# Optimization experiments

Measured on AMD Instinct MI355X. Metric: run time of the kernel, lower is better.

## Reference

```python
import jax, jax.numpy as jnp
import numpy as np

HEAD_SIZE = 1024
NUM_HEADS = 8
D_K = HEAD_SIZE // NUM_HEADS  # only used as the softmax scale; no head split in this module
B, S = 8, 2048


def setup_inputs() -> dict:
    key = jax.random.key(0)
    ks = jax.random.split(key, 11)
    d = HEAD_SIZE
    scale = 1.0 / np.sqrt(d)
    inp = {
        'query': jax.random.normal(ks[0], (B, S, d), dtype=jnp.float32),
        'key': jax.random.normal(ks[1], (B, S, d), dtype=jnp.float32),
        'value': jax.random.normal(ks[2], (B, S, d), dtype=jnp.float32),
        'Wq': jax.random.normal(ks[3], (d, d), dtype=jnp.float32) * scale,
        'bq': jnp.zeros((d,), dtype=jnp.float32),
        'Wk': jax.random.normal(ks[4], (d, d), dtype=jnp.float32) * scale,
        'bk': jnp.zeros((d,), dtype=jnp.float32),
        'Wv': jax.random.normal(ks[5], (d, d), dtype=jnp.float32) * scale,
        'bv': jnp.zeros((d,), dtype=jnp.float32),
        'Wo': jax.random.normal(ks[6], (d, d), dtype=jnp.float32) * scale,
        'bo': jnp.zeros((d,), dtype=jnp.float32),
    }
    return inp


def reference(query, key, value, Wq, bq, Wk, bk, Wv, bv, Wo, bo):
    # per-input linear projections (torch Linear: x @ W.T + b)
    q = jnp.einsum('bsd,ed->bse', query, Wq) + bq
    k = jnp.einsum('bsd,ed->bse', key, Wk) + bk
    v = jnp.einsum('bsd,ed->bse', value, Wv) + bv
    # NOTE: no head split in the original module; scale uses d_k = head_size/num_heads
    scores = jnp.einsum('bqd,bkd->bqk', q, k) / jnp.sqrt(jnp.float32(D_K))
    p_attn = jax.nn.softmax(scores, axis=-1)  # [B, S, S]
    x = jnp.einsum('bqk,bkd->bqd', p_attn, v)
    out = jnp.einsum('bsd,ed->bse', x, Wo) + bo
    return out
```

## Files before the change

kernel.cpp:

```cpp
#include <hip/hip_runtime.h>
#include <hip/hip_bf16.h>
#include <math.h>

typedef __bf16 bf16_t;
typedef _Float16 f16_t;
typedef bf16_t bf16x8 __attribute__((ext_vector_type(8)));
typedef bf16_t bf16x4 __attribute__((ext_vector_type(4)));
typedef f16_t  f16x8  __attribute__((ext_vector_type(8)));
typedef f16_t  f16x4  __attribute__((ext_vector_type(4)));
typedef float  f32x4  __attribute__((ext_vector_type(4)));

__global__ __launch_bounds__(256) void cvt_f32_bf16(
    const float* __restrict__ in, bf16_t* __restrict__ out, int n4) {
  int i = blockIdx.x * 256 + threadIdx.x;
  if (i >= n4) return;
  float4 v = ((const float4*)in)[i];
  bf16x4 o;
  o[0] = (bf16_t)v.x; o[1] = (bf16_t)v.y; o[2] = (bf16_t)v.z; o[3] = (bf16_t)v.w;
  ((bf16x4*)out)[i] = o;
}

__global__ __launch_bounds__(256) void transpose_bf16(
    const bf16_t* __restrict__ in, bf16_t* __restrict__ out, int R, int C) {
  __shared__ bf16_t t[64][65];
  size_t boff = (size_t)blockIdx.z * R * C;
  in += boff; out += boff;
  int r0 = blockIdx.y * 64, c0 = blockIdx.x * 64;
  int x = threadIdx.x & 63, y4 = threadIdx.x >> 6;
  #pragma unroll
  for (int yy = y4; yy < 64; yy += 4)
    t[yy][x] = in[(size_t)(r0 + yy) * C + c0 + x];
  __syncthreads();
  #pragma unroll
  for (int yy = y4; yy < 64; yy += 4)
    out[(size_t)(c0 + yy) * R + r0 + x] = t[x][yy];
}

__global__ __launch_bounds__(256) void softmax_rows_f16(f16_t* __restrict__ sc) {
  f16_t* rp = sc + (size_t)blockIdx.x * 2048;
  int tid = threadIdx.x;
  f16x8 v = ((const f16x8*)rp)[tid];
  float f[8];
  #pragma unroll
  for (int t = 0; t < 8; t++) f[t] = (float)v[t];

  float m = f[0];
  #pragma unroll
  for (int t = 1; t < 8; t++) m = fmaxf(m, f[t]);
  #pragma unroll
  for (int o = 32; o; o >>= 1) m = fmaxf(m, __shfl_xor(m, o));
  __shared__ float redm[4];
  if ((tid & 63) == 0) redm[tid >> 6] = m;
  __syncthreads();
  m = fmaxf(fmaxf(redm[0], redm[1]), fmaxf(redm[2], redm[3]));

  float s = 0.f;
  #pragma unroll
  for (int t = 0; t < 8; t++) { f[t] = __expf(f[t] - m); s += f[t]; }
  #pragma unroll
  for (int o = 32; o; o >>= 1) s += __shfl_xor(s, o);
  __shared__ float reds[4];
  if ((tid & 63) == 0) reds[tid >> 6] = s;
  __syncthreads();
  s = reds[0] + reds[1] + reds[2] + reds[3];
  float inv = 1.0f / s;

  bf16x8 o8;
  #pragma unroll
  for (int t = 0; t < 8; t++) o8[t] = (bf16_t)(f[t] * inv);
  ((bf16x8*)rp)[tid] = o8;
}

__device__ __forceinline__ void store4(float* p, float4 v) { *(float4*)p = v; }
__device__ __forceinline__ void store4(bf16_t* p, float4 v) {
  bf16x4 o; o[0] = (bf16_t)v.x; o[1] = (bf16_t)v.y;
  o[2] = (bf16_t)v.z; o[3] = (bf16_t)v.w; *(bf16x4*)p = o;
}
__device__ __forceinline__ void store4(f16_t* p, float4 v) {
  f16x4 o; o[0] = (f16_t)v.x; o[1] = (f16_t)v.y;
  o[2] = (f16_t)v.z; o[3] = (f16_t)v.w; *(f16x4*)p = o;
}

#define BM 256
#define BN 256
#define BK 64

__device__ __forceinline__ void load16_lds(const bf16_t* g, bf16_t* l) {
  __builtin_amdgcn_global_load_lds(
      (__attribute__((address_space(1))) void*)const_cast<bf16_t*>(g),
      (__attribute__((address_space(3))) void*)l, 16, 0, 0);
}

template <typename CT>
__global__ __launch_bounds__(512, 2) void gemm256(
    const bf16_t* __restrict__ A, int lda, size_t strA,
    const bf16_t* __restrict__ B, int ldb, size_t strB,
    CT* __restrict__ C, int ldc, size_t strC,
    const float* __restrict__ bias, float scale,
    int K, int batch_on_x) {
  __shared__ __align__(16) char smem[10][16384];
  char* smem0 = &smem[0][0];

  int bz, mt, nt;
  if (batch_on_x) { bz = blockIdx.x; nt = blockIdx.y; mt = blockIdx.z; }
  else            { mt = blockIdx.x; nt = blockIdx.y; bz = blockIdx.z; }
  A += (size_t)bz * strA;
  B += (size_t)bz * strB;
  C += (size_t)bz * strC;
  int m0 = mt * BM, n0 = nt * BN;
  int tid  = threadIdx.x;
  int lane = tid & 63, wv = tid >> 6;
  int wrow = wv >> 2;
  int wcol = wv & 3;

  f32x4 acc[8][4];
  #pragma unroll
  for (int i = 0; i < 8; i++)
    #pragma unroll
    for (int j = 0; j < 4; j++) acc[i][j] = (f32x4)0.f;

  int lrow = lane & 15;
  int lk8  = (lane >> 4) * 8;
  int xm   = (lrow & 8) << 2;

  auto rd = [&](const char* half, int blk, int kcol) -> bf16x8 {
    int byte = (((blk << 1) + (kcol >> 5)) << 10)
             + (lrow << 6) + (((kcol & 31) << 1) ^ xm);
    return *(const bf16x8*)(half + byte);
  };

  auto stage_half = [&](int h, int slot) {
    int th = h >> 2, hf = h & 3;
    char* dstb = smem0 + slot * 16384;
    const bf16_t* g; int rb, ld;
    if (hf < 2) { g = A; rb = m0 + hf * 128;       ld = lda; }
    else        { g = B; rb = n0 + (hf - 2) * 128; ld = ldb; }
    int k0 = th * BK;
    #pragma unroll
    for (int q = 0; q < 2; q++) {
      int l = q * 8192 + wv * 1024 + lane * 16;
      int inner = l & 1023, s = l >> 10;
      int rl   = ((s >> 1) << 4) | (inner >> 6);
      int colb = (inner & 63) ^ (((inner >> 9) & 1) << 5);
      int col  = ((s & 1) << 5) | (colb >> 1);
      load16_lds(g + (size_t)(rb + rl) * ld + k0 + col,
                 (bf16_t*)(dstb + q * 8192 + wv * 1024));
    }
  };

  int nk = K / BK;
  int nh = 4 * nk;
  int bl = (wcol & 1) * 4;

  #pragma unroll
  for (int h = 0; h < 8; ++h)
    if (h < nh) stage_half(h, h);
  asm volatile("s_waitcnt vmcnt(8)" ::: "memory");
  asm volatile("s_barrier" ::: "memory");

  bf16x8 a0[4][2], a1[4][2], bb[2][2];
  {
    const char* Ah0 = smem0 + (0 + wrow) * 16384;
    const char* Bh0 = smem0 + (2 + (wcol >> 1)) * 16384;
    #pragma unroll
    for (int i = 0; i < 4; ++i)
      #pragma unroll
      for (int s = 0; s < 2; ++s)
        a0[i][s] = rd(Ah0, i, s * 32 + lk8);
    #pragma unroll
    for (int j = 0; j < 2; ++j)
      #pragma unroll
      for (int s = 0; s < 2; ++s)
        bb[j][s] = rd(Bh0, bl + j, s * 32 + lk8);
  }

  int rs = 0;
  int ss = 8;

  for (int t = 0; t < nk; ++t) {
    int hb = 4 * t + 8;
    int sa  = rs + wrow;
    int sb  = rs + 2 + (wcol >> 1); if (sb  >= 10) sb  -= 10;
    int san = rs + 4 + wrow;        if (san >= 10) san -= 10;
    int sbn = rs + 6 + (wcol >> 1); if (sbn >= 10) sbn -= 10;
    const char* Ah  = smem0 + sa  * 16384;
    const char* Bh  = smem0 + sb  * 16384;
    const char* Ahn = smem0 + san * 16384;
    const char* Bhn = smem0 + sbn * 16384;

    #pragma unroll
    for (int i = 0; i < 4; ++i)
      #pragma unroll
      for (int s = 0; s < 2; ++s)
        a1[i][s] = rd(Ah, 4 + i, s * 32 + lk8);
    if (hb + 0 < nh) { stage_half(hb + 0, ss); ss = (ss == 9) ? 0 : ss + 1; }
    asm volatile("s_barrier" ::: "memory");
    __builtin_amdgcn_s_setprio(1);
    #pragma unroll
    for (int i = 0; i < 4; ++i)
      #pragma unroll
      for (int j = 0; j < 2; ++j)
        #pragma unroll
        for (int s = 0; s < 2; ++s)
          acc[i][j] = __builtin_amdgcn_mfma_f32_16x16x32_bf16(
              a0[i][s], bb[j][s], acc[i][j], 0, 0, 0);
    __builtin_amdgcn_s_setprio(0);
    asm volatile("s_barrier" ::: "memory");

    if (hb + 1 < nh) { stage_half(hb + 1, ss); ss = (ss == 9) ? 0 : ss + 1; }
    asm volatile("s_barrier" ::: "memory");
    __builtin_amdgcn_s_setprio(1);
    #pragma unroll
    for (int i = 0; i < 4; ++i)
      #pragma unroll
      for (int j = 0; j < 2; ++j)
        #pragma unroll
        for (int s = 0; s < 2; ++s)
          acc[4 + i][j] = __builtin_amdgcn_mfma_f32_16x16x32_bf16(
              a1[i][s], bb[j][s], acc[4 + i][j], 0, 0, 0);
    __builtin_amdgcn_s_setprio(0);
    asm volatile("s_barrier" ::: "memory");

    #pragma unroll
    for (int j = 0; j < 2; ++j)
      #pragma unroll
      for (int s = 0; s < 2; ++s)
        bb[j][s] = rd(Bh, bl + 2 + j, s * 32 + lk8);
    if (hb + 2 < nh) { stage_half(hb + 2, ss); ss = (ss == 9) ? 0 : ss + 1; }
    if (t <= nk - 3) asm volatile("s_waitcnt vmcnt(6)" ::: "memory");
    else             asm volatile("s_waitcnt vmcnt(0)" ::: "memory");
    asm volatile("s_barrier" ::: "memory");
    __builtin_amdgcn_s_setprio(1);
    #pragma unroll
    for (int i = 0; i < 4; ++i)
      #pragma unroll
      for (int j = 0; j < 2; ++j)
        #pragma unroll
        for (int s = 0; s < 2; ++s)
          acc[4 + i][2 + j] = __builtin_amdgcn_mfma_f32_16x16x32_bf16(
              a1[i][s], bb[j][s], acc[4 + i][2 + j], 0, 0, 0);
    __builtin_amdgcn_s_setprio(0);
    asm volatile("s_barrier" ::: "memory");

    if (hb + 3 < nh) { stage_half(hb + 3, ss); ss = (ss == 9) ? 0 : ss + 1; }
    asm volatile("s_barrier" ::: "memory");
    __builtin_amdgcn_s_setprio(1);
    #pragma unroll
    for (int i = 0; i < 4; ++i)
      #pragma unroll
      for (int j = 0; j < 2; ++j)
        #pragma unroll
        for (int s = 0; s < 2; ++s)
          acc[i][2 + j] = __builtin_amdgcn_mfma_f32_16x16x32_bf16(
              a0[i][s], bb[j][s], acc[i][2 + j], 0, 0, 0);
    __builtin_amdgcn_s_setprio(0);
    if (t + 1 < nk) {
      #pragma unroll
      for (int j = 0; j < 2; ++j)
        #pragma unroll
        for (int s = 0; s < 2; ++s)
          bb[j][s] = rd(Bhn, bl + j, s * 32 + lk8);
      #pragma unroll
      for (int i = 0; i < 4; ++i)
        #pragma unroll
        for (int s = 0; s < 2; ++s)
          a0[i][s] = rd(Ahn, i, s * 32 + lk8);
    }
    asm volatile("s_barrier" ::: "memory");

    rs += 4; if (rs >= 10) rs -= 10;
  }

  float* Cs = (float*)smem0;
  #pragma unroll
  for (int q = 0; q < 4; ++q) {
    __syncthreads();
    if (wrow == (q >> 1)) {
      #pragma unroll
      for (int ii = 0; ii < 4; ++ii) {
        int i = (q & 1) * 4 + ii;
        int lr = ii * 16 + (lane >> 4) * 4;
        #pragma unroll
        for (int j = 0; j < 4; ++j) {
          int lc = wcol * 64 + j * 16 + (lane & 15);
          #pragma unroll
          for (int r = 0; r < 4; ++r)
            Cs[(lr + r) * 260 + lc] = acc[i][j][r];
        }
      }
    }
    __syncthreads();
    #pragma unroll
    for (int io = 0; io < 8; ++io) {
      int idx = io * 512 + tid;
      int r = idx >> 6, c4 = (idx & 63) * 4;
      float4 v = *(const float4*)&Cs[r * 260 + c4];
      int grow = m0 + q * 64 + r;
      int gcol = n0 + c4;
      float4 bv = bias ? *(const float4*)&bias[gcol] : make_float4(0, 0, 0, 0);
      v.x = v.x * scale + bv.x; v.y = v.y * scale + bv.y;
      v.z = v.z * scale + bv.z; v.w = v.w * scale + bv.w;
      store4(C + (size_t)grow * ldc + gcol, v);
    }
  }
}

extern "C" void kernel_launch(void* const* d_in, const int* in_sizes, int n_in,
                              void* d_out, int out_size, void* d_ws, size_t ws_size,
                              hipStream_t stream) {
  const float* query = (const float*)d_in[0];
  const float* key_  = (const float*)d_in[1];
  const float* value = (const float*)d_in[2];
  const float* Wq = (const float*)d_in[3];
  const float* bq = (const float*)d_in[4];
  const float* Wk = (const float*)d_in[5];
  const float* bk = (const float*)d_in[6];
  const float* Wv = (const float*)d_in[7];
  const float* bv = (const float*)d_in[8];
  const float* Wo = (const float*)d_in[9];
  const float* bo = (const float*)d_in[10];
  float* out = (float*)d_out;

  const int Bb = 8, S = 2048, D = 1024;
  const int MS = Bb * S;
  const size_t ND = (size_t)MS * D;
  const size_t WD = (size_t)D * D;

  char* ws = (char*)d_ws;
  bf16_t* Wqb = (bf16_t*)ws;
  bf16_t* Wkb = Wqb + WD;
  bf16_t* Wvb = Wkb + WD;
  bf16_t* Wob = Wvb + WD;
  f16_t*  SC  = (f16_t*)(Wob + WD);
  bf16_t* IN  = (bf16_t*)SC;
  bf16_t* Qb  = (bf16_t*)((char*)SC + (size_t)Bb * S * S * 2);
  bf16_t* Kb  = Qb + ND;
  bf16_t* VT  = Kb;
  bf16_t* Xb  = Kb + ND;

  const int n4i = (int)(ND / 4), n4w = (int)(WD / 4);
  dim3 blk(512);

  cvt_f32_bf16<<<dim3(n4w / 256), 256, 0, stream>>>(Wq, Wqb, n4w);
  cvt_f32_bf16<<<dim3(n4w / 256), 256, 0, stream>>>(Wk, Wkb, n4w);
  cvt_f32_bf16<<<dim3(n4w / 256), 256, 0, stream>>>(Wv, Wvb, n4w);
  cvt_f32_bf16<<<dim3(n4w / 256), 256, 0, stream>>>(Wo, Wob, n4w);

  dim3 pgrid(MS / BM, D / BN, 1);
  cvt_f32_bf16<<<dim3(n4i / 256), 256, 0, stream>>>(query, IN, n4i);
  gemm256<bf16_t><<<pgrid, blk, 0, stream>>>(
      IN, D, 0, Wqb, D, 0, Qb, D, 0, bq, 1.f, D, 0);
  cvt_f32_bf16<<<dim3(n4i / 256), 256, 0, stream>>>(key_, IN, n4i);
  gemm256<bf16_t><<<pgrid, blk, 0, stream>>>(
      IN, D, 0, Wkb, D, 0, Kb, D, 0, bk, 1.f, D, 0);
  cvt_f32_bf16<<<dim3(n4i / 256), 256, 0, stream>>>(value, IN, n4i);
  gemm256<bf16_t><<<pgrid, blk, 0, stream>>>(
      IN, D, 0, Wvb, D, 0, Xb, D, 0, bv, 1.f, D, 0);

  gemm256<f16_t><<<dim3(Bb, S / BN, S / BM), blk, 0, stream>>>(
      Qb, D, (size_t)S * D, Kb, D, (size_t)S * D, SC, S, (size_t)S * S,
      nullptr, 0.08838834764831845f, D, 1);

  transpose_bf16<<<dim3(D / 64, S / 64, Bb), 256, 0, stream>>>(Xb, VT, S, D);

  softmax_rows_f16<<<dim3(Bb * S), 256, 0, stream>>>(SC);

  gemm256<bf16_t><<<dim3(Bb, D / BN, S / BM), blk, 0, stream>>>(
      (const bf16_t*)SC, S, (size_t)S * S, VT, S, (size_t)D * S,
      Xb, D, (size_t)S * D, nullptr, 1.f, S, 1);

  gemm256<float><<<pgrid, blk, 0, stream>>>(
      Xb, D, 0, Wob, D, 0, out, D, 0, bo, 1.f, D, 0);
}
```

Before: 572.9 us.

## Fuse fp32-to-bf16 input conversion and V transpose into projection GEMMs

The projection GEMMs now load fp32 activations straight from global memory into registers, convert them to bf16 and write them into LDS. This removes the three separate conversion kernels and their round trips through a bf16 workspace. The V projection writes its output transposed from the epilogue, which removes the separate transpose kernel, and the four weight conversions are merged into one launch. In exchange, A-tile staging now goes through registers instead of direct-to-LDS loads, which adds register pressure and changes the pipeline wait counts. The transposed epilogue also does strided reads from shared memory.

```diff
diff --git a/kernel.cpp b/kernel.cpp
--- a/kernel.cpp
+++ b/kernel.cpp
@@ -10,30 +10,18 @@
 typedef f16_t  f16x4  __attribute__((ext_vector_type(4)));
 typedef float  f32x4  __attribute__((ext_vector_type(4)));
 
-__global__ __launch_bounds__(256) void cvt_f32_bf16(
-    const float* __restrict__ in, bf16_t* __restrict__ out, int n4) {
+__global__ __launch_bounds__(256) void cvt_w4(
+    const float* __restrict__ w0, const float* __restrict__ w1,
+    const float* __restrict__ w2, const float* __restrict__ w3,
+    bf16_t* __restrict__ out, int n4) {
+  const float* src = blockIdx.y == 0 ? w0 : blockIdx.y == 1 ? w1
+                   : blockIdx.y == 2 ? w2 : w3;
   int i = blockIdx.x * 256 + threadIdx.x;
   if (i >= n4) return;
-  float4 v = ((const float4*)in)[i];
+  float4 v = ((const float4*)src)[i];
   bf16x4 o;
   o[0] = (bf16_t)v.x; o[1] = (bf16_t)v.y; o[2] = (bf16_t)v.z; o[3] = (bf16_t)v.w;
-  ((bf16x4*)out)[i] = o;
-}
-
-__global__ __launch_bounds__(256) void transpose_bf16(
-    const bf16_t* __restrict__ in, bf16_t* __restrict__ out, int R, int C) {
-  __shared__ bf16_t t[64][65];
-  size_t boff = (size_t)blockIdx.z * R * C;
-  in += boff; out += boff;
-  int r0 = blockIdx.y * 64, c0 = blockIdx.x * 64;
-  int x = threadIdx.x & 63, y4 = threadIdx.x >> 6;
-  #pragma unroll
-  for (int yy = y4; yy < 64; yy += 4)
-    t[yy][x] = in[(size_t)(r0 + yy) * C + c0 + x];
-  __syncthreads();
-  #pragma unroll
-  for (int yy = y4; yy < 64; yy += 4)
-    out[(size_t)(c0 + yy) * R + r0 + x] = t[x][yy];
+  ((bf16x4*)(out + (size_t)blockIdx.y * n4 * 4))[i] = o;
 }
 
 __global__ __launch_bounds__(256) void softmax_rows_f16(f16_t* __restrict__ sc) {
@@ -91,9 +79,9 @@
       (__attribute__((address_space(3))) void*)l, 16, 0, 0);
 }
 
-template <typename CT>
+template <typename CT, bool AF32, bool TOUT>
 __global__ __launch_bounds__(512, 2) void gemm256(
-    const bf16_t* __restrict__ A, int lda, size_t strA,
+    const void* __restrict__ Av, int lda, size_t strA,
     const bf16_t* __restrict__ B, int ldb, size_t strB,
     CT* __restrict__ C, int ldc, size_t strC,
     const float* __restrict__ bias, float scale,
@@ -104,7 +92,8 @@
   int bz, mt, nt;
   if (batch_on_x) { bz = blockIdx.x; nt = blockIdx.y; mt = blockIdx.z; }
   else            { mt = blockIdx.x; nt = blockIdx.y; bz = blockIdx.z; }
-  A += (size_t)bz * strA;
+  const bf16_t* A16 = (const bf16_t*)Av + (AF32 ? 0 : (size_t)bz * strA);
+  const float*  A32 = (const float*)Av + (AF32 ? (size_t)bz * strA : 0);
   B += (size_t)bz * strB;
   C += (size_t)bz * strC;
   int m0 = mt * BM, n0 = nt * BN;
@@ -129,13 +118,8 @@
     return *(const bf16x8*)(half + byte);
   };
 
-  auto stage_half = [&](int h, int slot) {
-    int th = h >> 2, hf = h & 3;
+  auto stage_g = [&](const bf16_t* g, int rb, int ld, int k0, int slot) {
     char* dstb = smem0 + slot * 16384;
-    const bf16_t* g; int rb, ld;
-    if (hf < 2) { g = A; rb = m0 + hf * 128;       ld = lda; }
-    else        { g = B; rb = n0 + (hf - 2) * 128; ld = ldb; }
-    int k0 = th * BK;
     #pragma unroll
     for (int q = 0; q < 2; q++) {
       int l = q * 8192 + wv * 1024 + lane * 16;
@@ -148,15 +132,69 @@
     }
   };
 
+  auto ldA32 = [&](int th, int hf, f32x4* r) {
+    #pragma unroll
+    for (int q = 0; q < 2; q++) {
+      int sub  = q * 8 + wv;
+      int grow = hf * 128 + (sub >> 1) * 16 + (lane >> 2);
+      int gcol = (sub & 1) * 32 + (lane & 3) * 8;
+      const float* gp = A32 + (size_t)(m0 + grow) * lda + th * BK + gcol;
+      r[2 * q]     = *(const f32x4*)gp;
+      r[2 * q + 1] = *(const f32x4*)(gp + 4);
+    }
+  };
+  auto wrA = [&](const f32x4* r, int slot) {
+    char* db = smem0 + slot * 16384;
+    #pragma unroll
+    for (int q = 0; q < 2; q++) {
+      int dl  = q * 8192 + wv * 1024 + lane * 16;
+      int dst = dl ^ (((dl >> 9) & 1) << 5);
+      bf16x8 o;
+      #pragma unroll
+      for (int e = 0; e < 4; e++) {
+        o[e]     = (bf16_t)r[2 * q][e];
+        o[4 + e] = (bf16_t)r[2 * q + 1][e];
+      }
+      *(bf16x8*)(db + dst) = o;
+    }
+  };
+
   int nk = K / BK;
-  int nh = 4 * nk;
   int bl = (wcol & 1) * 4;
 
-  #pragma unroll
-  for (int h = 0; h < 8; ++h)
-    if (h < nh) stage_half(h, h);
-  asm volatile("s_waitcnt vmcnt(8)" ::: "memory");
-  asm volatile("s_barrier" ::: "memory");
+  f32x4 rA0[4], rA1[4];
+
+  if constexpr (AF32) {
+    f32x4 rP[4][4];
+    #pragma unroll
+    for (int tt = 0; tt < 2; ++tt)
+      #pragma unroll
+      for (int hf = 0; hf < 2; ++hf)
+        if (tt < nk) ldA32(tt, hf, rP[tt * 2 + hf]);
+    #pragma unroll
+    for (int tt = 0; tt < 2; ++tt)
+      #pragma unroll
+      for (int hf = 0; hf < 2; ++hf)
+        if (tt < nk) stage_g(B, n0 + hf * 128, ldb, tt * BK, tt * 4 + 2 + hf);
+    #pragma unroll
+    for (int tt = 0; tt < 2; ++tt)
+      #pragma unroll
+      for (int hf = 0; hf < 2; ++hf)
+        if (tt < nk) wrA(rP[tt * 2 + hf], tt * 4 + hf);
+    asm volatile("s_waitcnt vmcnt(4)" ::: "memory");
+    asm volatile("s_waitcnt lgkmcnt(0)" ::: "memory");
+    asm volatile("s_barrier" ::: "memory");
+  } else {
+    #pragma unroll
+    for (int h = 0; h < 8; ++h)
+      if (h < 4 * nk) {
+        int th = h >> 2, hf = h & 3;
+        if (hf < 2) stage_g(A16, m0 + hf * 128, lda, th * BK, h);
+        else        stage_g(B, n0 + (hf - 2) * 128, ldb, th * BK, h);
+      }
+    asm volatile("s_waitcnt vmcnt(8)" ::: "memory");
+    asm volatile("s_barrier" ::: "memory");
+  }
 
   bf16x8 a0[4][2], a1[4][2], bb[2][2];
   {
@@ -178,7 +216,11 @@
   int ss = 8;
 
   for (int t = 0; t < nk; ++t) {
-    int hb = 4 * t + 8;
+    bool do_stage = (t + 2 < nk);
+    int s0 = ss;
+    int s1 = ss + 1; if (s1 >= 10) s1 -= 10;
+    int s2 = ss + 2; if (s2 >= 10) s2 -= 10;
+    int s3 = ss + 3; if (s3 >= 10) s3 -= 10;
     int sa  = rs + wrow;
     int sb  = rs + 2 + (wcol >> 1); if (sb  >= 10) sb  -= 10;
     int san = rs + 4 + wrow;        if (san >= 10) san -= 10;
@@ -193,7 +235,10 @@
       #pragma unroll
       for (int s = 0; s < 2; ++s)
         a1[i][s] = rd(Ah, 4 + i, s * 32 + lk8);
-    if (hb + 0 < nh) { stage_half(hb + 0, ss); ss = (ss == 9) ? 0 : ss + 1; }
+    if (do_stage) {
+      if constexpr (AF32) ldA32(t + 2, 0, rA0);
+      else                stage_g(A16, m0, lda, (t + 2) * BK, s0);
+    }
     asm volatile("s_barrier" ::: "memory");
     __builtin_amdgcn_s_setprio(1);
     #pragma unroll
@@ -207,7 +252,10 @@
     __builtin_amdgcn_s_setprio(0);
     asm volatile("s_barrier" ::: "memory");
 
-    if (hb + 1 < nh) { stage_half(hb + 1, ss); ss = (ss == 9) ? 0 : ss + 1; }
+    if (do_stage) {
+      if constexpr (AF32) ldA32(t + 2, 1, rA1);
+      else                stage_g(A16, m0 + 128, lda, (t + 2) * BK, s1);
+    }
     asm volatile("s_barrier" ::: "memory");
     __builtin_amdgcn_s_setprio(1);
     #pragma unroll
@@ -226,9 +274,14 @@
       #pragma unroll
       for (int s = 0; s < 2; ++s)
         bb[j][s] = rd(Bh, bl + 2 + j, s * 32 + lk8);
-    if (hb + 2 < nh) { stage_half(hb + 2, ss); ss = (ss == 9) ? 0 : ss + 1; }
-    if (t <= nk - 3) asm volatile("s_waitcnt vmcnt(6)" ::: "memory");
-    else             asm volatile("s_waitcnt vmcnt(0)" ::: "memory");
+    if (do_stage) stage_g(B, n0, ldb, (t + 2) * BK, s2);
+    if constexpr (AF32) {
+      if (t <= nk - 3) asm volatile("s_waitcnt vmcnt(10)" ::: "memory");
+      else             asm volatile("s_waitcnt vmcnt(0)" ::: "memory");
+    } else {
+      if (t <= nk - 3) asm volatile("s_waitcnt vmcnt(6)" ::: "memory");
+      else             asm volatile("s_waitcnt vmcnt(0)" ::: "memory");
+    }
     asm volatile("s_barrier" ::: "memory");
     __builtin_amdgcn_s_setprio(1);
     #pragma unroll
@@ -242,7 +295,7 @@
     __builtin_amdgcn_s_setprio(0);
     asm volatile("s_barrier" ::: "memory");
 
-    if (hb + 3 < nh) { stage_half(hb + 3, ss); ss = (ss == 9) ? 0 : ss + 1; }
+    if (do_stage) stage_g(B, n0 + 128, ldb, (t + 2) * BK, s3);
     asm volatile("s_barrier" ::: "memory");
     __builtin_amdgcn_s_setprio(1);
     #pragma unroll
@@ -254,6 +307,9 @@
           acc[i][2 + j] = __builtin_amdgcn_mfma_f32_16x16x32_bf16(
               a0[i][s], bb[j][s], acc[i][2 + j], 0, 0, 0);
     __builtin_amdgcn_s_setprio(0);
+    if constexpr (AF32) {
+      if (do_stage) { wrA(rA0, s0); wrA(rA1, s1); }
+    }
     if (t + 1 < nk) {
       #pragma unroll
       for (int j = 0; j < 2; ++j)
@@ -268,6 +324,7 @@
     }
     asm volatile("s_barrier" ::: "memory");
 
+    if (do_stage) { ss += 4; if (ss >= 10) ss -= 10; }
     rs += 4; if (rs >= 10) rs -= 10;
   }
 
@@ -290,17 +347,34 @@
       }
     }
     __syncthreads();
-    #pragma unroll
-    for (int io = 0; io < 8; ++io) {
-      int idx = io * 512 + tid;
-      int r = idx >> 6, c4 = (idx & 63) * 4;
-      float4 v = *(const float4*)&Cs[r * 260 + c4];
-      int grow = m0 + q * 64 + r;
-      int gcol = n0 + c4;
-      float4 bv = bias ? *(const float4*)&bias[gcol] : make_float4(0, 0, 0, 0);
-      v.x = v.x * scale + bv.x; v.y = v.y * scale + bv.y;
-      v.z = v.z * scale + bv.z; v.w = v.w * scale + bv.w;
-      store4(C + (size_t)grow * ldc + gcol, v);
+    if constexpr (TOUT) {
+      int n = tid & 255, mh = tid >> 8;
+      int mbase = m0 + q * 64 + mh * 32;
+      int NN = gridDim.y * BN;
+      float bvn = bias ? bias[n0 + n] : 0.f;
+      CT* dst = C + (size_t)(mbase >> 11) * (size_t)NN * ldc
+                  + (size_t)(n0 + n) * ldc + (mbase & 2047);
+      #pragma unroll
+      for (int g = 0; g < 4; ++g) {
+        bf16x8 o;
+        #pragma unroll
+        for (int e = 0; e < 8; ++e)
+          o[e] = (bf16_t)(Cs[(mh * 32 + g * 8 + e) * 260 + n] * scale + bvn);
+        *(bf16x8*)(dst + g * 8) = o;
+      }
+    } else {
+      #pragma unroll
+      for (int io = 0; io < 8; ++io) {
+        int idx = io * 512 + tid;
+        int r = idx >> 6, c4 = (idx & 63) * 4;
+        float4 v = *(const float4*)&Cs[r * 260 + c4];
+        int grow = m0 + q * 64 + r;
+        int gcol = n0 + c4;
+        float4 bv = bias ? *(const float4*)&bias[gcol] : make_float4(0, 0, 0, 0);
+        v.x = v.x * scale + bv.x; v.y = v.y * scale + bv.y;
+        v.z = v.z * scale + bv.z; v.w = v.w * scale + bv.w;
+        store4(C + (size_t)grow * ldc + gcol, v);
+      }
     }
   }
 }
@@ -332,43 +406,35 @@
   bf16_t* Wvb = Wkb + WD;
   bf16_t* Wob = Wvb + WD;
   f16_t*  SC  = (f16_t*)(Wob + WD);
-  bf16_t* IN  = (bf16_t*)SC;
   bf16_t* Qb  = (bf16_t*)((char*)SC + (size_t)Bb * S * S * 2);
   bf16_t* Kb  = Qb + ND;
   bf16_t* VT  = Kb;
   bf16_t* Xb  = Kb + ND;
 
-  const int n4i = (int)(ND / 4), n4w = (int)(WD / 4);
+  const int n4w = (int)(WD / 4);
   dim3 blk(512);
-
-  cvt_f32_bf16<<<dim3(n4w / 256), 256, 0, stream>>>(Wq, Wqb, n4w);
-  cvt_f32_bf16<<<dim3(n4w / 256), 256, 0, stream>>>(Wk, Wkb, n4w);
-  cvt_f32_bf16<<<dim3(n4w / 256), 256, 0, stream>>>(Wv, Wvb, n4w);
-  cvt_f32_bf16<<<dim3(n4w / 256), 256, 0, stream>>>(Wo, Wob, n4w);
-
   dim3 pgrid(MS / BM, D / BN, 1);
-  cvt_f32_bf16<<<dim3(n4i / 256), 256, 0, stream>>>(query, IN, n4i);
-  gemm256<bf16_t><<<pgrid, blk, 0, stream>>>(
-      IN, D, 0, Wqb, D, 0, Qb, D, 0, bq, 1.f, D, 0);
-  cvt_f32_bf16<<<dim3(n4i / 256), 256, 0, stream>>>(key_, IN, n4i);
-  gemm256<bf16_t><<<pgrid, blk, 0, stream>>>(
-      IN, D, 0, Wkb, D, 0, Kb, D, 0, bk, 1.f, D, 0);
-  cvt_f32_bf16<<<dim3(n4i / 256), 256, 0, stream>>>(value, IN, n4i);
-  gemm256<bf16_t><<<pgrid, blk, 0, stream>>>(
-      IN, D, 0, Wvb, D, 0, Xb, D, 0, bv, 1.f, D, 0);
-
-  gemm256<f16_t><<<dim3(Bb, S / BN, S / BM), blk, 0, stream>>>(
+
+  cvt_w4<<<dim3(n4w / 256, 4), 256, 0, stream>>>(Wq, Wk, Wv, Wo, Wqb, n4w);
+
+  gemm256<bf16_t, true, false><<<pgrid, blk, 0, stream>>>(
+      query, D, 0, Wqb, D, 0, Qb, D, 0, bq, 1.f, D, 0);
+  gemm256<bf16_t, true, false><<<pgrid, blk, 0, stream>>>(
+      key_, D, 0, Wkb, D, 0, Kb, D, 0, bk, 1.f, D, 0);
+
+  gemm256<f16_t, false, false><<<dim3(Bb, S / BN, S / BM), blk, 0, stream>>>(
       Qb, D, (size_t)S * D, Kb, D, (size_t)S * D, SC, S, (size_t)S * S,
       nullptr, 0.08838834764831845f, D, 1);
 
-  transpose_bf16<<<dim3(D / 64, S / 64, Bb), 256, 0, stream>>>(Xb, VT, S, D);
+  gemm256<bf16_t, true, true><<<pgrid, blk, 0, stream>>>(
+      value, D, 0, Wvb, D, 0, VT, S , 0, bv, 1.f, D, 0);
 
   softmax_rows_f16<<<dim3(Bb * S), 256, 0, stream>>>(SC);
 
-  gemm256<bf16_t><<<dim3(Bb, D / BN, S / BM), blk, 0, stream>>>(
+  gemm256<bf16_t, false, false><<<dim3(Bb, D / BN, S / BM), blk, 0, stream>>>(
       (const bf16_t*)SC, S, (size_t)S * S, VT, S, (size_t)D * S,
       Xb, D, (size_t)S * D, nullptr, 1.f, S, 1);
 
-  gemm256<float><<<pgrid, blk, 0, stream>>>(
+  gemm256<float, false, false><<<pgrid, blk, 0, stream>>>(
       Xb, D, 0, Wob, D, 0, out, D, 0, bo, 1.f, D, 0);
 }
```

Measured after the change: 635.0 us. 10.8% more time.
